# Kernel optimization log

Hardware: AMD Instinct MI355X
Metric: run time of the kernel (lower is better)

The kernel has to match this reference:

```python
import jax, jax.numpy as jnp
import numpy as np

B, N, K = 2, 65536, 16
D_OUT, D_FEAT = 64, 64
EPS = 1e-6


def setup_inputs() -> dict:
    key = jax.random.key(0)
    ks = jax.random.split(key, 8)
    coords = jax.random.normal(ks[0], (B, N, 3), dtype=jnp.float32)
    features = jax.random.normal(ks[1], (B, D_FEAT, N, 1), dtype=jnp.float32)
    knn_points = jax.random.randint(ks[2], (B, N, K), 0, N)
    knn_dist = jax.random.uniform(ks[3], (B, N, K), dtype=jnp.float32)
    # SharedMLP params: 1x1 Conv2d(10 -> D_OUT) + BatchNorm2d(D_OUT)
    W = jax.random.normal(ks[4], (D_OUT, 10), dtype=jnp.float32) * 0.1
    b = jnp.zeros((D_OUT,), dtype=jnp.float32)
    gamma = jnp.ones((D_OUT,), dtype=jnp.float32)
    beta = jnp.zeros((D_OUT,), dtype=jnp.float32)
    return {"coords": coords, "features": features, "knn_points": knn_points,
            "knn_dist": knn_dist, "W": W, "b": b, "gamma": gamma, "beta": beta}


def reference(coords, features, knn_points, knn_dist, W, b, gamma, beta):
    Bd, Nd, Kd = knn_points.shape
    # gather neighbor xyz: neighbors[b,n,k,:] = coords[b, knn_points[b,n,k], :]
    nb = jax.vmap(lambda c, i: c[i])(coords, knn_points)          # [B,N,K,3]
    nb = jnp.transpose(nb, (0, 3, 1, 2))                          # [B,3,N,K]
    center = jnp.broadcast_to(
        jnp.transpose(coords, (0, 2, 1))[..., None], (Bd, 3, Nd, Kd))  # [B,3,N,K]
    # 10-channel spatial encoding: xyz, neighbor xyz, relative xyz, distance
    sp = jnp.concatenate([center, nb, center - nb, knn_dist[:, None]], axis=1)  # [B,10,N,K]
    # 1x1 conv
    x = jnp.einsum('oc,bcnk->bonk', W, sp) + b[None, :, None, None]  # [B,D_OUT,N,K]
    # BatchNorm2d in training mode: batch statistics over (B,N,K) per channel
    mean = x.mean(axis=(0, 2, 3))
    var = x.var(axis=(0, 2, 3))
    x = (x - mean[None, :, None, None]) * jax.lax.rsqrt(var + EPS)[None, :, None, None]
    x = x * gamma[None, :, None, None] + beta[None, :, None, None]
    x = jax.nn.relu(x)
    feat = jnp.broadcast_to(features, (Bd, features.shape[1], Nd, Kd))
    return jnp.concatenate([x, feat], axis=1)  # [B, D_OUT+D_FEAT, N, K]
```

## Files before the change

kernel.cpp:

```cpp
#include <hip/hip_runtime.h>
#include <hip/hip_bf16.h>

#define N_PTS 65536
#define BATCH 2
#define KNN   16
#define NBLK_S2 2048
#define NBLK_V1 512

typedef float float4n __attribute__((ext_vector_type(4)));

__device__ __forceinline__ int tri(int i, int j) {
    return i * 7 - (i * (i - 1)) / 2 + (j - i);
}

__global__ __launch_bounds__(256) void k_featstats(const float* __restrict__ feat,
                                                   float* __restrict__ out,
                                                   const float* __restrict__ coords,
                                                   const int* __restrict__ knn,
                                                   const float* __restrict__ dist,
                                                   float* __restrict__ partials) {
    int bid = blockIdx.x;
    if (bid < NBLK_S2) {
        int gid = bid * 256 + threadIdx.x;
        int q  = gid & 3;
        int pp = gid >> 2;
        int b  = pp >> 16;
        const float* cp = coords + (size_t)pp * 3;
        float cx = cp[0], cy = cp[1], cz = cp[2];
        const float* cb = coords + (size_t)b * (N_PTS * 3);

        int4   ia = *(const int4*)  (knn  + ((size_t)pp << 4) + (q << 2));
        float4 da = *(const float4*)(dist + ((size_t)pp << 4) + (q << 2));
        int   idx[4] = {ia.x, ia.y, ia.z, ia.w};
        float dd[4]  = {da.x, da.y, da.z, da.w};

        float Gx = 0.f, Gy = 0.f, Gz = 0.f, D1 = 0.f, D2 = 0.f;
        float Sxx = 0.f, Sxy = 0.f, Sxz = 0.f, Syy = 0.f, Syz = 0.f, Szz = 0.f;
        float NDx = 0.f, NDy = 0.f, NDz = 0.f;
#pragma unroll
        for (int k = 0; k < 4; k++) {
            const float* qq = cb + (size_t)idx[k] * 3;
            float nx = qq[0], ny = qq[1], nz = qq[2], d = dd[k];
            Gx += nx; Gy += ny; Gz += nz; D1 += d; D2 += d * d;
            Sxx += nx * nx; Sxy += nx * ny; Sxz += nx * nz;
            Syy += ny * ny; Syz += ny * nz; Szz += nz * nz;
            NDx += nx * d; NDy += ny * d; NDz += nz * d;
        }

        __shared__ float red[4][35];
        int lane = threadIdx.x & 63, wid = threadIdx.x >> 6;
        int slot = 0;
#define RED1(expr) { float v_ = (expr); \
        v_ += __shfl_xor(v_, 32); v_ += __shfl_xor(v_, 16); \
        v_ += __shfl_xor(v_, 8);  v_ += __shfl_xor(v_, 4);  \
        v_ += __shfl_xor(v_, 2);  v_ += __shfl_xor(v_, 1);  \
        if (lane == 0) red[wid][slot] = v_; slot++; }
        RED1(4.f*cx) RED1(4.f*cy) RED1(4.f*cz) RED1(Gx) RED1(Gy) RED1(Gz) RED1(D1)
        RED1(4.f*cx*cx) RED1(4.f*cx*cy) RED1(4.f*cx*cz)
        RED1(cx*Gx) RED1(cx*Gy) RED1(cx*Gz) RED1(cx*D1)
        RED1(4.f*cy*cy) RED1(4.f*cy*cz)
        RED1(cy*Gx) RED1(cy*Gy) RED1(cy*Gz) RED1(cy*D1)
        RED1(4.f*cz*cz)
        RED1(cz*Gx) RED1(cz*Gy) RED1(cz*Gz) RED1(cz*D1)
        RED1(Sxx) RED1(Sxy) RED1(Sxz) RED1(NDx)
        RED1(Syy) RED1(Syz) RED1(NDy)
        RED1(Szz) RED1(NDz)
        RED1(D2)
#undef RED1
        __syncthreads();
        if (threadIdx.x < 35) {
            int i = threadIdx.x;
            partials[i * NBLK_S2 + bid] =
                (red[0][i] + red[1][i]) + (red[2][i] + red[3][i]);
        }
    } else {
        int gid = (bid - NBLK_S2) * 256 + threadIdx.x;
        int q4 = gid & 3;
        int r  = gid >> 2;
        float v = feat[r];
        int b = r >> 22;
        int f = (r >> 16) & 63;
        int n = r & 0xFFFF;
        size_t base = (((size_t)b * 128 + 64 + f) * N_PTS + n) * KNN + (q4 << 2);
        float4n vv = {v, v, v, v};
        __builtin_nontemporal_store(vv, reinterpret_cast<float4n*>(out + base));
    }
}

__global__ __launch_bounds__(256) void k_prep256(const float* __restrict__ W,
                                                 const float* __restrict__ bias,
                                                 const float* __restrict__ gamma,
                                                 const float* __restrict__ beta,
                                                 const float* __restrict__ partials,
                                                 float* __restrict__ w8) {
    __shared__ float red[4][35];
    __shared__ float sst[35];
    int t = threadIdx.x;
    float acc[35];
    const float* p0 = partials + t * 8;
#pragma unroll
    for (int i = 0; i < 35; i++) {
        const float* p = p0 + i * NBLK_S2;
        float4 a = *(const float4*)p;
        float4 c = *(const float4*)(p + 4);
        acc[i] = ((a.x + a.y) + (a.z + a.w)) + ((c.x + c.y) + (c.z + c.w));
    }
    int lane = t & 63, wid = t >> 6;
#pragma unroll
    for (int i = 0; i < 35; i++) {
        float v = acc[i];
#pragma unroll
        for (int off = 32; off; off >>= 1) v += __shfl_xor(v, off);
        if (lane == 0) red[wid][i] = v;
    }
    __syncthreads();
    if (t < 35) sst[t] = (red[0][t] + red[1][t]) + (red[2][t] + red[3][t]);
    __syncthreads();

    if (t >= 64) return;
    int o = t;
    const float invM = 1.0f / (float)((size_t)BATCH * N_PTS * KNN);
    float m[7];
#pragma unroll
    for (int j = 0; j < 7; j++) m[j] = sst[j] * invM;
    const float* Wo = W + o * 10;
    float wv[7];
    wv[0] = Wo[0] + Wo[6]; wv[1] = Wo[1] + Wo[7]; wv[2] = Wo[2] + Wo[8];
    wv[3] = Wo[3] - Wo[6]; wv[4] = Wo[4] - Wo[7]; wv[5] = Wo[5] - Wo[8];
    wv[6] = Wo[9];
    float mean = bias[o];
#pragma unroll
    for (int j = 0; j < 7; j++) mean += wv[j] * m[j];
    float var = 0.f;
#pragma unroll
    for (int i = 0; i < 7; i++) {
#pragma unroll
        for (int j = 0; j < 7; j++) {
            int a = i < j ? i : j, c = i < j ? j : i;
            float cov = sst[7 + tri(a, c)] * invM - m[i] * m[j];
            var += wv[i] * wv[j] * cov;
        }
    }
    float s = gamma[o] * rsqrtf(var + 1e-6f);
    float sh = beta[o] - mean * s;
#pragma unroll
    for (int j = 0; j < 7; j++) w8[o * 8 + j] = s * wv[j];
    w8[o * 8 + 7] = s * bias[o] + sh;
}

__global__ __launch_bounds__(256) void k_stats_fb(const float* __restrict__ coords,
                                                  const int* __restrict__ knn,
                                                  const float* __restrict__ dist,
                                                  float* __restrict__ stats_atomic,
                                                  float* __restrict__ partials,
                                                  int use_part) {
    int gid = blockIdx.x * 256 + threadIdx.x;
    int b = gid >> 16;
    const float* cp = coords + (size_t)gid * 3;
    float cx = cp[0], cy = cp[1], cz = cp[2];
    const float* cb = coords + (size_t)b * (N_PTS * 3);
    const int* ip = knn + ((size_t)gid << 4);
    const float* dp = dist + ((size_t)gid << 4);

    float s[35];
#pragma unroll
    for (int i = 0; i < 35; i++) s[i] = 0.f;
    for (int k = 0; k < KNN; k++) {
        int idx = ip[k];
        const float* q = cb + (size_t)idx * 3;
        float v[7];
        v[0] = cx; v[1] = cy; v[2] = cz;
        v[3] = q[0]; v[4] = q[1]; v[5] = q[2];
        v[6] = dp[k];
        int t = 7;
#pragma unroll
        for (int i = 0; i < 7; i++) {
            s[i] += v[i];
#pragma unroll
            for (int j = i; j < 7; j++) { s[t] += v[i] * v[j]; t++; }
        }
    }
    __shared__ float red[4][35];
    int lane = threadIdx.x & 63;
    int wid  = threadIdx.x >> 6;
#pragma unroll
    for (int i = 0; i < 35; i++) {
        float v = s[i];
#pragma unroll
        for (int off = 32; off; off >>= 1) v += __shfl_xor(v, off);
        if (lane == 0) red[wid][i] = v;
    }
    __syncthreads();
    if (threadIdx.x < 35) {
        int i = threadIdx.x;
        float v = (red[0][i] + red[1][i]) + (red[2][i] + red[3][i]);
        if (use_part) partials[i * NBLK_V1 + blockIdx.x] = v;
        else          atomicAdd(&stats_atomic[i], v);
    }
}

__global__ __launch_bounds__(64) void k_prep_fb(const float* __restrict__ W,
                                                const float* __restrict__ bias,
                                                const float* __restrict__ gamma,
                                                const float* __restrict__ beta,
                                                const float* __restrict__ stats_atomic,
                                                const float* __restrict__ partials,
                                                int use_part,
                                                float* __restrict__ w8) {
    __shared__ float sst[35];
    int t = threadIdx.x;
    if (t < 35) {
        if (use_part) {
            const float* p = partials + t * NBLK_V1;
            float a0 = 0.f, a1 = 0.f, a2 = 0.f, a3 = 0.f;
            for (int j = 0; j < NBLK_V1; j += 4) {
                a0 += p[j]; a1 += p[j + 1]; a2 += p[j + 2]; a3 += p[j + 3];
            }
            sst[t] = (a0 + a1) + (a2 + a3);
        } else {
            sst[t] = stats_atomic[t];
        }
    }
    __syncthreads();
    int o = t;
    const float invM = 1.0f / (float)((size_t)BATCH * N_PTS * KNN);
    float m[7];
#pragma unroll
    for (int j = 0; j < 7; j++) m[j] = sst[j] * invM;
    const float* Wo = W + o * 10;
    float wv[7];
    wv[0] = Wo[0] + Wo[6]; wv[1] = Wo[1] + Wo[7]; wv[2] = Wo[2] + Wo[8];
    wv[3] = Wo[3] - Wo[6]; wv[4] = Wo[4] - Wo[7]; wv[5] = Wo[5] - Wo[8];
    wv[6] = Wo[9];
    float mean = bias[o];
#pragma unroll
    for (int j = 0; j < 7; j++) mean += wv[j] * m[j];
    float var = 0.f;
#pragma unroll
    for (int i = 0; i < 7; i++) {
#pragma unroll
        for (int j = 0; j < 7; j++) {
            int a = i < j ? i : j, c = i < j ? j : i;
            float cov = sst[7 + tri(a, c)] * invM - m[i] * m[j];
            var += wv[i] * wv[j] * cov;
        }
    }
    float s = gamma[o] * rsqrtf(var + 1e-6f);
    float sh = beta[o] - mean * s;
#pragma unroll
    for (int j = 0; j < 7; j++) w8[o * 8 + j] = s * wv[j];
    w8[o * 8 + 7] = s * bias[o] + sh;
}

__global__ __launch_bounds__(256) void k_feat(const float* __restrict__ feat,
                                              float* __restrict__ out) {
    int gid = blockIdx.x * 256 + threadIdx.x;
    int q4 = gid & 3;
    int r  = gid >> 2;
    float v = feat[r];
    int b = r >> 22;
    int f = (r >> 16) & 63;
    int n = r & 0xFFFF;
    size_t base = (((size_t)b * 128 + 64 + f) * N_PTS + n) * KNN + (q4 << 2);
    float4n vv = {v, v, v, v};
    __builtin_nontemporal_store(vv, reinterpret_cast<float4n*>(out + base));
}

__global__ __launch_bounds__(256) void k_x(const float* __restrict__ coords,
                                           const int* __restrict__ knn,
                                           const float* __restrict__ dist,
                                           const float* __restrict__ w8g,
                                           float* __restrict__ out) {
    __shared__ float w8[512];
    for (int i = threadIdx.x; i < 512; i += 256) w8[i] = w8g[i];
    __syncthreads();

    int gid = blockIdx.x * 256 + threadIdx.x;
    int q  = gid & 3;
    int pp = gid >> 2;
    int b = pp >> 16;
    int n = pp & 0xFFFF;

    const float* cp = coords + (size_t)pp * 3;
    float cx = cp[0], cy = cp[1], cz = cp[2];
    const float* cb = coords + (size_t)b * (N_PTS * 3);

    int4   ia = *(const int4*)  (knn  + ((size_t)pp << 4) + (q << 2));
    float4 da = *(const float4*)(dist + ((size_t)pp << 4) + (q << 2));
    int   idx[4] = {ia.x, ia.y, ia.z, ia.w};
    float dd[4]  = {da.x, da.y, da.z, da.w};
    float nx[4], ny[4], nz[4];
#pragma unroll
    for (int k = 0; k < 4; k++) {
        const float* qq = cb + (size_t)idx[k] * 3;
        nx[k] = qq[0]; ny[k] = qq[1]; nz[k] = qq[2];
    }

    size_t base = ((size_t)b * 128) * (N_PTS * KNN) + (size_t)n * KNN + (q << 2);
#pragma unroll 4
    for (int c = 0; c < 64; c++) {
        float4 wa = *reinterpret_cast<const float4*>(&w8[c << 3]);
        float4 wb = *reinterpret_cast<const float4*>(&w8[(c << 3) + 4]);
        float s0 = fmaf(cx, wa.x, fmaf(cy, wa.y, fmaf(cz, wa.z, wb.w)));
        float x[4];
#pragma unroll
        for (int k = 0; k < 4; k++) {
            float v = fmaf(dd[k], wb.z, fmaf(nz[k], wb.y, fmaf(ny[k], wb.x, fmaf(nx[k], wa.w, s0))));
            x[k] = fmaxf(v, 0.f);
        }
        float4n v0 = {x[0], x[1], x[2], x[3]};
        __builtin_nontemporal_store(v0,
            reinterpret_cast<float4n*>(out + base + (size_t)c * (N_PTS * KNN)));
    }
}

extern "C" void kernel_launch(void* const* d_in, const int* in_sizes, int n_in,
                              void* d_out, int out_size, void* d_ws, size_t ws_size,
                              hipStream_t stream) {
    const float* coords   = (const float*)d_in[0];
    const float* features = (const float*)d_in[1];
    const int*   knn      = (const int*)d_in[2];
    const float* dist     = (const float*)d_in[3];
    const float* W        = (const float*)d_in[4];
    const float* bias     = (const float*)d_in[5];
    const float* gamma    = (const float*)d_in[6];
    const float* beta     = (const float*)d_in[7];
    float* out            = (float*)d_out;

    float* stats    = (float*)d_ws;
    float* w8       = stats + 64;
    float* partials = w8 + 512;
    size_t need2 = (64 + 512 + 35 * NBLK_S2) * sizeof(float);
    size_t need1 = (64 + 512 + 35 * NBLK_V1) * sizeof(float);

    if (ws_size >= need2) {
        k_featstats<<<NBLK_S2 + 131072, 256, 0, stream>>>(features, out, coords, knn, dist,
                                                          partials);
        k_prep256<<<1, 256, 0, stream>>>(W, bias, gamma, beta, partials, w8);
    } else {
        int use_part = (ws_size >= need1) ? 1 : 0;
        if (!use_part)
            (void)hipMemsetAsync(d_ws, 0, 64 * sizeof(float), stream);
        k_stats_fb<<<NBLK_V1, 256, 0, stream>>>(coords, knn, dist, stats, partials, use_part);
        k_prep_fb<<<1, 64, 0, stream>>>(W, bias, gamma, beta, stats, partials, use_part, w8);
        k_feat<<<131072, 256, 0, stream>>>(features, out);
    }
    k_x<<<2048, 256, 0, stream>>>(coords, knn, dist, w8, out);
}
```

Measured before the change: 232.1 us.

## Stage neighbor data in shared memory and split output channels across waves

The output-writing kernel now handles 128 points per block instead of 64. It stages the gathered neighbor xyz plus distance and the center coords into LDS, and then each wave writes 16 of the 64 channels for all 128 points. The aim is to make each wave's stores to a channel plane contiguous over a larger span and to cut register pressure. The cost is an extra LDS round trip, a barrier, and a 36KB shared footprint that may limit occupancy.

```diff
diff --git a/kernel.cpp b/kernel.cpp
--- a/kernel.cpp
+++ b/kernel.cpp
@@ -266,51 +266,72 @@
     __builtin_nontemporal_store(vv, reinterpret_cast<float4n*>(out + base));
 }
 
-__global__ __launch_bounds__(256) void k_x(const float* __restrict__ coords,
-                                           const int* __restrict__ knn,
-                                           const float* __restrict__ dist,
-                                           const float* __restrict__ w8g,
-                                           float* __restrict__ out) {
-    __shared__ float w8[512];
-    for (int i = threadIdx.x; i < 512; i += 256) w8[i] = w8g[i];
-    __syncthreads();
-
-    int gid = blockIdx.x * 256 + threadIdx.x;
-    int q  = gid & 3;
-    int pp = gid >> 2;
-    int b = pp >> 16;
-    int n = pp & 0xFFFF;
-
-    const float* cp = coords + (size_t)pp * 3;
-    float cx = cp[0], cy = cp[1], cz = cp[2];
+__global__ __launch_bounds__(256) void k_x2(const float* __restrict__ coords,
+                                            const int* __restrict__ knn,
+                                            const float* __restrict__ dist,
+                                            const float* __restrict__ w8g,
+                                            float* __restrict__ out) {
+    __shared__ float4n sp2[2048];
+    __shared__ float4n cxy[128];
+    __shared__ float   w8[512];
+
+    int tid = threadIdx.x;
+    int pp0 = blockIdx.x * 128;
+    int b   = pp0 >> 16;
     const float* cb = coords + (size_t)b * (N_PTS * 3);
 
-    int4   ia = *(const int4*)  (knn  + ((size_t)pp << 4) + (q << 2));
-    float4 da = *(const float4*)(dist + ((size_t)pp << 4) + (q << 2));
-    int   idx[4] = {ia.x, ia.y, ia.z, ia.w};
-    float dd[4]  = {da.x, da.y, da.z, da.w};
-    float nx[4], ny[4], nz[4];
-#pragma unroll
-    for (int k = 0; k < 4; k++) {
-        const float* qq = cb + (size_t)idx[k] * 3;
-        nx[k] = qq[0]; ny[k] = qq[1]; nz[k] = qq[2];
-    }
-
-    size_t base = ((size_t)b * 128) * (N_PTS * KNN) + (size_t)n * KNN + (q << 2);
-#pragma unroll 4
-    for (int c = 0; c < 64; c++) {
+    for (int i = tid; i < 512; i += 256) w8[i] = w8g[i];
+    if (tid < 128) {
+        const float* cp = coords + (size_t)(pp0 + tid) * 3;
+        float4n c = {cp[0], cp[1], cp[2], 0.f};
+        cxy[tid] = c;
+    }
+#pragma unroll
+    for (int s = 0; s < 2; s++) {
+        int Q  = tid + s * 256;
+        int pt = Q >> 2, q = Q & 3;
+        int pp = pp0 + pt;
+        int4   ia = *(const int4*)  (knn  + ((size_t)pp << 4) + (q << 2));
+        float4 da = *(const float4*)(dist + ((size_t)pp << 4) + (q << 2));
+        int   idx[4] = {ia.x, ia.y, ia.z, ia.w};
+        float dd[4]  = {da.x, da.y, da.z, da.w};
+        int base = ((pt >> 4) * 4) * 64 + (pt & 15) * 4 + q;
+#pragma unroll
+        for (int kk = 0; kk < 4; kk++) {
+            const float* qq = cb + (size_t)idx[kk] * 3;
+            float4n v = {qq[0], qq[1], qq[2], dd[kk]};
+            sp2[base + kk * 64] = v;
+        }
+    }
+    __syncthreads();
+
+    int lane = tid & 63, wv = tid >> 6;
+    int q = lane & 3, ptl = lane >> 2;
+    int n0 = pp0 & 0xFFFF;
+    const size_t CS = (size_t)N_PTS * KNN;
+    float* outp = out + ((size_t)b * 128) * CS + (size_t)n0 * KNN;
+
+    for (int ci = 0; ci < 16; ci++) {
+        int c = wv * 16 + ci;
         float4 wa = *reinterpret_cast<const float4*>(&w8[c << 3]);
         float4 wb = *reinterpret_cast<const float4*>(&w8[(c << 3) + 4]);
-        float s0 = fmaf(cx, wa.x, fmaf(cy, wa.y, fmaf(cz, wa.z, wb.w)));
-        float x[4];
-#pragma unroll
-        for (int k = 0; k < 4; k++) {
-            float v = fmaf(dd[k], wb.z, fmaf(nz[k], wb.y, fmaf(ny[k], wb.x, fmaf(nx[k], wa.w, s0))));
-            x[k] = fmaxf(v, 0.f);
-        }
-        float4n v0 = {x[0], x[1], x[2], x[3]};
-        __builtin_nontemporal_store(v0,
-            reinterpret_cast<float4n*>(out + base + (size_t)c * (N_PTS * KNN)));
+        float* oc = outp + (size_t)c * CS;
+#pragma unroll
+        for (int j = 0; j < 8; j++) {
+            int pt = j * 16 + ptl;
+            float4n cc = cxy[pt];
+            float s0 = fmaf(cc.x, wa.x, fmaf(cc.y, wa.y, fmaf(cc.z, wa.z, wb.w)));
+            float x[4];
+#pragma unroll
+            for (int kk = 0; kk < 4; kk++) {
+                float4n v = sp2[(j * 4 + kk) * 64 + lane];
+                x[kk] = fmaxf(fmaf(v.w, wb.z, fmaf(v.z, wb.y,
+                              fmaf(v.y, wb.x, fmaf(v.x, wa.w, s0)))), 0.f);
+            }
+            float4n o = {x[0], x[1], x[2], x[3]};
+            __builtin_nontemporal_store(o,
+                reinterpret_cast<float4n*>(oc + (pt << 4) + (q << 2)));
+        }
     }
 }
 
@@ -345,5 +366,5 @@
         k_prep_fb<<<1, 64, 0, stream>>>(W, bias, gamma, beta, stats, partials, use_part, w8);
         k_feat<<<131072, 256, 0, stream>>>(features, out);
     }
-    k_x<<<2048, 256, 0, stream>>>(coords, knn, dist, w8, out);
-}
+    k_x2<<<(BATCH * N_PTS) / 128, 256, 0, stream>>>(coords, knn, dist, w8, out);
+}
```

Result: faster. 217.4 us (median of 2 runs) (-6.3%).

## Move feature broadcast from stats kernel into interleaved x/feature write kernel

Applied to the files above, without the earlier changes.

The feature broadcast blocks are taken out of the statistics kernel, which is now small. They are merged with the conv/BN/ReLU output kernel into one launch where every 65th block computes x and the other 64 broadcast features. This interleaves the compute-heavy x blocks with the pure-store feature blocks so both write streams share bandwidth in one pass, and it removes the fallback path's separate k_feat launch. The cost is that all feature writes now wait behind the stats and prep kernels, and each block pays a div/mod by 65 plus a branch.

```diff
diff --git a/kernel.cpp b/kernel.cpp
--- a/kernel.cpp
+++ b/kernel.cpp
@@ -13,77 +13,62 @@
     return i * 7 - (i * (i - 1)) / 2 + (j - i);
 }
 
-__global__ __launch_bounds__(256) void k_featstats(const float* __restrict__ feat,
-                                                   float* __restrict__ out,
-                                                   const float* __restrict__ coords,
-                                                   const int* __restrict__ knn,
-                                                   const float* __restrict__ dist,
-                                                   float* __restrict__ partials) {
+__global__ __launch_bounds__(256) void k_stats4L(const float* __restrict__ coords,
+                                                 const int* __restrict__ knn,
+                                                 const float* __restrict__ dist,
+                                                 float* __restrict__ partials) {
     int bid = blockIdx.x;
-    if (bid < NBLK_S2) {
-        int gid = bid * 256 + threadIdx.x;
-        int q  = gid & 3;
-        int pp = gid >> 2;
-        int b  = pp >> 16;
-        const float* cp = coords + (size_t)pp * 3;
-        float cx = cp[0], cy = cp[1], cz = cp[2];
-        const float* cb = coords + (size_t)b * (N_PTS * 3);
-
-        int4   ia = *(const int4*)  (knn  + ((size_t)pp << 4) + (q << 2));
-        float4 da = *(const float4*)(dist + ((size_t)pp << 4) + (q << 2));
-        int   idx[4] = {ia.x, ia.y, ia.z, ia.w};
-        float dd[4]  = {da.x, da.y, da.z, da.w};
-
-        float Gx = 0.f, Gy = 0.f, Gz = 0.f, D1 = 0.f, D2 = 0.f;
-        float Sxx = 0.f, Sxy = 0.f, Sxz = 0.f, Syy = 0.f, Syz = 0.f, Szz = 0.f;
-        float NDx = 0.f, NDy = 0.f, NDz = 0.f;
-#pragma unroll
-        for (int k = 0; k < 4; k++) {
-            const float* qq = cb + (size_t)idx[k] * 3;
-            float nx = qq[0], ny = qq[1], nz = qq[2], d = dd[k];
-            Gx += nx; Gy += ny; Gz += nz; D1 += d; D2 += d * d;
-            Sxx += nx * nx; Sxy += nx * ny; Sxz += nx * nz;
-            Syy += ny * ny; Syz += ny * nz; Szz += nz * nz;
-            NDx += nx * d; NDy += ny * d; NDz += nz * d;
-        }
-
-        __shared__ float red[4][35];
-        int lane = threadIdx.x & 63, wid = threadIdx.x >> 6;
-        int slot = 0;
+    int gid = bid * 256 + threadIdx.x;
+    int q  = gid & 3;
+    int pp = gid >> 2;
+    int b  = pp >> 16;
+    const float* cp = coords + (size_t)pp * 3;
+    float cx = cp[0], cy = cp[1], cz = cp[2];
+    const float* cb = coords + (size_t)b * (N_PTS * 3);
+
+    int4   ia = *(const int4*)  (knn  + ((size_t)pp << 4) + (q << 2));
+    float4 da = *(const float4*)(dist + ((size_t)pp << 4) + (q << 2));
+    int   idx[4] = {ia.x, ia.y, ia.z, ia.w};
+    float dd[4]  = {da.x, da.y, da.z, da.w};
+
+    float Gx = 0.f, Gy = 0.f, Gz = 0.f, D1 = 0.f, D2 = 0.f;
+    float Sxx = 0.f, Sxy = 0.f, Sxz = 0.f, Syy = 0.f, Syz = 0.f, Szz = 0.f;
+    float NDx = 0.f, NDy = 0.f, NDz = 0.f;
+#pragma unroll
+    for (int k = 0; k < 4; k++) {
+        const float* qq = cb + (size_t)idx[k] * 3;
+        float nx = qq[0], ny = qq[1], nz = qq[2], d = dd[k];
+        Gx += nx; Gy += ny; Gz += nz; D1 += d; D2 += d * d;
+        Sxx += nx * nx; Sxy += nx * ny; Sxz += nx * nz;
+        Syy += ny * ny; Syz += ny * nz; Szz += nz * nz;
+        NDx += nx * d; NDy += ny * d; NDz += nz * d;
+    }
+
+    __shared__ float red[4][35];
+    int lane = threadIdx.x & 63, wid = threadIdx.x >> 6;
+    int slot = 0;
 #define RED1(expr) { float v_ = (expr); \
-        v_ += __shfl_xor(v_, 32); v_ += __shfl_xor(v_, 16); \
-        v_ += __shfl_xor(v_, 8);  v_ += __shfl_xor(v_, 4);  \
-        v_ += __shfl_xor(v_, 2);  v_ += __shfl_xor(v_, 1);  \
-        if (lane == 0) red[wid][slot] = v_; slot++; }
-        RED1(4.f*cx) RED1(4.f*cy) RED1(4.f*cz) RED1(Gx) RED1(Gy) RED1(Gz) RED1(D1)
-        RED1(4.f*cx*cx) RED1(4.f*cx*cy) RED1(4.f*cx*cz)
-        RED1(cx*Gx) RED1(cx*Gy) RED1(cx*Gz) RED1(cx*D1)
-        RED1(4.f*cy*cy) RED1(4.f*cy*cz)
-        RED1(cy*Gx) RED1(cy*Gy) RED1(cy*Gz) RED1(cy*D1)
-        RED1(4.f*cz*cz)
-        RED1(cz*Gx) RED1(cz*Gy) RED1(cz*Gz) RED1(cz*D1)
-        RED1(Sxx) RED1(Sxy) RED1(Sxz) RED1(NDx)
-        RED1(Syy) RED1(Syz) RED1(NDy)
-        RED1(Szz) RED1(NDz)
-        RED1(D2)
+    v_ += __shfl_xor(v_, 32); v_ += __shfl_xor(v_, 16); \
+    v_ += __shfl_xor(v_, 8);  v_ += __shfl_xor(v_, 4);  \
+    v_ += __shfl_xor(v_, 2);  v_ += __shfl_xor(v_, 1);  \
+    if (lane == 0) red[wid][slot] = v_; slot++; }
+    RED1(4.f*cx) RED1(4.f*cy) RED1(4.f*cz) RED1(Gx) RED1(Gy) RED1(Gz) RED1(D1)
+    RED1(4.f*cx*cx) RED1(4.f*cx*cy) RED1(4.f*cx*cz)
+    RED1(cx*Gx) RED1(cx*Gy) RED1(cx*Gz) RED1(cx*D1)
+    RED1(4.f*cy*cy) RED1(4.f*cy*cz)
+    RED1(cy*Gx) RED1(cy*Gy) RED1(cy*Gz) RED1(cy*D1)
+    RED1(4.f*cz*cz)
+    RED1(cz*Gx) RED1(cz*Gy) RED1(cz*Gz) RED1(cz*D1)
+    RED1(Sxx) RED1(Sxy) RED1(Sxz) RED1(NDx)
+    RED1(Syy) RED1(Syz) RED1(NDy)
+    RED1(Szz) RED1(NDz)
+    RED1(D2)
 #undef RED1
-        __syncthreads();
-        if (threadIdx.x < 35) {
-            int i = threadIdx.x;
-            partials[i * NBLK_S2 + bid] =
-                (red[0][i] + red[1][i]) + (red[2][i] + red[3][i]);
-        }
-    } else {
-        int gid = (bid - NBLK_S2) * 256 + threadIdx.x;
-        int q4 = gid & 3;
-        int r  = gid >> 2;
-        float v = feat[r];
-        int b = r >> 22;
-        int f = (r >> 16) & 63;
-        int n = r & 0xFFFF;
-        size_t base = (((size_t)b * 128 + 64 + f) * N_PTS + n) * KNN + (q4 << 2);
-        float4n vv = {v, v, v, v};
-        __builtin_nontemporal_store(vv, reinterpret_cast<float4n*>(out + base));
+    __syncthreads();
+    if (threadIdx.x < 35) {
+        int i = threadIdx.x;
+        partials[i * NBLK_S2 + bid] =
+            (red[0][i] + red[1][i]) + (red[2][i] + red[3][i]);
     }
 }
 
@@ -252,65 +237,67 @@
     w8[o * 8 + 7] = s * bias[o] + sh;
 }
 
-__global__ __launch_bounds__(256) void k_feat(const float* __restrict__ feat,
-                                              float* __restrict__ out) {
-    int gid = blockIdx.x * 256 + threadIdx.x;
-    int q4 = gid & 3;
-    int r  = gid >> 2;
-    float v = feat[r];
-    int b = r >> 22;
-    int f = (r >> 16) & 63;
-    int n = r & 0xFFFF;
-    size_t base = (((size_t)b * 128 + 64 + f) * N_PTS + n) * KNN + (q4 << 2);
-    float4n vv = {v, v, v, v};
-    __builtin_nontemporal_store(vv, reinterpret_cast<float4n*>(out + base));
-}
-
-__global__ __launch_bounds__(256) void k_x(const float* __restrict__ coords,
-                                           const int* __restrict__ knn,
-                                           const float* __restrict__ dist,
-                                           const float* __restrict__ w8g,
-                                           float* __restrict__ out) {
-    __shared__ float w8[512];
-    for (int i = threadIdx.x; i < 512; i += 256) w8[i] = w8g[i];
-    __syncthreads();
-
-    int gid = blockIdx.x * 256 + threadIdx.x;
-    int q  = gid & 3;
-    int pp = gid >> 2;
-    int b = pp >> 16;
-    int n = pp & 0xFFFF;
-
-    const float* cp = coords + (size_t)pp * 3;
-    float cx = cp[0], cy = cp[1], cz = cp[2];
-    const float* cb = coords + (size_t)b * (N_PTS * 3);
-
-    int4   ia = *(const int4*)  (knn  + ((size_t)pp << 4) + (q << 2));
-    float4 da = *(const float4*)(dist + ((size_t)pp << 4) + (q << 2));
-    int   idx[4] = {ia.x, ia.y, ia.z, ia.w};
-    float dd[4]  = {da.x, da.y, da.z, da.w};
-    float nx[4], ny[4], nz[4];
-#pragma unroll
-    for (int k = 0; k < 4; k++) {
-        const float* qq = cb + (size_t)idx[k] * 3;
-        nx[k] = qq[0]; ny[k] = qq[1]; nz[k] = qq[2];
-    }
-
-    size_t base = ((size_t)b * 128) * (N_PTS * KNN) + (size_t)n * KNN + (q << 2);
+__global__ __launch_bounds__(256, 8) void k_xfeat(const float* __restrict__ feat,
+                                                  const float* __restrict__ coords,
+                                                  const int* __restrict__ knn,
+                                                  const float* __restrict__ dist,
+                                                  const float* __restrict__ w8g,
+                                                  float* __restrict__ out) {
+    int bid = blockIdx.x;
+    int q65 = bid / 65, r65 = bid % 65;
+    if (r65 == 64) {
+        __shared__ float w8[512];
+        for (int i = threadIdx.x; i < 512; i += 256) w8[i] = w8g[i];
+        __syncthreads();
+
+        int gid = q65 * 256 + threadIdx.x;
+        int q  = gid & 3;
+        int pp = gid >> 2;
+        int b = pp >> 16;
+        int n = pp & 0xFFFF;
+
+        const float* cp = coords + (size_t)pp * 3;
+        float cx = cp[0], cy = cp[1], cz = cp[2];
+        const float* cb = coords + (size_t)b * (N_PTS * 3);
+
+        int4   ia = *(const int4*)  (knn  + ((size_t)pp << 4) + (q << 2));
+        float4 da = *(const float4*)(dist + ((size_t)pp << 4) + (q << 2));
+        int   idx[4] = {ia.x, ia.y, ia.z, ia.w};
+        float dd[4]  = {da.x, da.y, da.z, da.w};
+        float nx[4], ny[4], nz[4];
+#pragma unroll
+        for (int k = 0; k < 4; k++) {
+            const float* qq = cb + (size_t)idx[k] * 3;
+            nx[k] = qq[0]; ny[k] = qq[1]; nz[k] = qq[2];
+        }
+
+        size_t base = ((size_t)b * 128) * (N_PTS * KNN) + (size_t)n * KNN + (q << 2);
 #pragma unroll 4
-    for (int c = 0; c < 64; c++) {
-        float4 wa = *reinterpret_cast<const float4*>(&w8[c << 3]);
-        float4 wb = *reinterpret_cast<const float4*>(&w8[(c << 3) + 4]);
-        float s0 = fmaf(cx, wa.x, fmaf(cy, wa.y, fmaf(cz, wa.z, wb.w)));
-        float x[4];
-#pragma unroll
-        for (int k = 0; k < 4; k++) {
-            float v = fmaf(dd[k], wb.z, fmaf(nz[k], wb.y, fmaf(ny[k], wb.x, fmaf(nx[k], wa.w, s0))));
-            x[k] = fmaxf(v, 0.f);
-        }
-        float4n v0 = {x[0], x[1], x[2], x[3]};
-        __builtin_nontemporal_store(v0,
-            reinterpret_cast<float4n*>(out + base + (size_t)c * (N_PTS * KNN)));
+        for (int c = 0; c < 64; c++) {
+            float4 wa = *reinterpret_cast<const float4*>(&w8[c << 3]);
+            float4 wb = *reinterpret_cast<const float4*>(&w8[(c << 3) + 4]);
+            float s0 = fmaf(cx, wa.x, fmaf(cy, wa.y, fmaf(cz, wa.z, wb.w)));
+            float x[4];
+#pragma unroll
+            for (int k = 0; k < 4; k++) {
+                float v = fmaf(dd[k], wb.z, fmaf(nz[k], wb.y, fmaf(ny[k], wb.x, fmaf(nx[k], wa.w, s0))));
+                x[k] = fmaxf(v, 0.f);
+            }
+            float4n v0 = {x[0], x[1], x[2], x[3]};
+            __builtin_nontemporal_store(v0,
+                reinterpret_cast<float4n*>(out + base + (size_t)c * (N_PTS * KNN)));
+        }
+    } else {
+        int gid = (q65 * 64 + r65) * 256 + threadIdx.x;
+        int q4 = gid & 3;
+        int r  = gid >> 2;
+        float v = feat[r];
+        int b = r >> 22;
+        int f = (r >> 16) & 63;
+        int n = r & 0xFFFF;
+        size_t base = (((size_t)b * 128 + 64 + f) * N_PTS + n) * KNN + (q4 << 2);
+        float4n vv = {v, v, v, v};
+        __builtin_nontemporal_store(vv, reinterpret_cast<float4n*>(out + base));
     }
 }
 
@@ -334,8 +321,7 @@
     size_t need1 = (64 + 512 + 35 * NBLK_V1) * sizeof(float);
 
     if (ws_size >= need2) {
-        k_featstats<<<NBLK_S2 + 131072, 256, 0, stream>>>(features, out, coords, knn, dist,
-                                                          partials);
+        k_stats4L<<<NBLK_S2, 256, 0, stream>>>(coords, knn, dist, partials);
         k_prep256<<<1, 256, 0, stream>>>(W, bias, gamma, beta, partials, w8);
     } else {
         int use_part = (ws_size >= need1) ? 1 : 0;
@@ -343,7 +329,6 @@
             (void)hipMemsetAsync(d_ws, 0, 64 * sizeof(float), stream);
         k_stats_fb<<<NBLK_V1, 256, 0, stream>>>(coords, knn, dist, stats, partials, use_part);
         k_prep_fb<<<1, 64, 0, stream>>>(W, bias, gamma, beta, stats, partials, use_part, w8);
-        k_feat<<<131072, 256, 0, stream>>>(features, out);
-    }
-    k_x<<<2048, 256, 0, stream>>>(coords, knn, dist, w8, out);
-}
+    }
+    k_xfeat<<<133120, 256, 0, stream>>>(features, coords, knn, dist, w8, out);
+}
```

Measured after the change: 240.2 us. 1.03x slower.
